# Kernel optimization log

Hardware: AMD Instinct MI355X
Metric: run time of the kernel (lower is better)

The kernel has to match this reference:

```python
import jax, jax.numpy as jnp
import numpy as np

NUM_NODES = 10000
WINDOW = 8
IN_C = 8
HID = 64
N_TOT = WINDOW * NUM_NODES
N_EDGES = 1280000
EPS = 1e-5


def setup_inputs() -> dict:
    key = jax.random.key(0)
    ks = jax.random.split(key, 12)
    s = 0.05
    X = jax.random.normal(ks[0], (N_TOT, IN_C), jnp.float32)
    edge_index = jax.random.randint(ks[1], (2, N_EDGES), 0, N_TOT, dtype=jnp.int32)
    edge_weight = jax.random.uniform(ks[2], (N_EDGES,), jnp.float32)
    return dict(
        X=X, edge_index=edge_index, edge_weight=edge_weight,
        w1=jax.random.normal(ks[3], (IN_C, HID), jnp.float32) * s, b1=jnp.zeros(HID, jnp.float32),
        w2=jax.random.normal(ks[4], (HID, HID), jnp.float32) * s, b2=jnp.zeros(HID, jnp.float32),
        g1=jnp.ones(HID, jnp.float32), be1=jnp.zeros(HID, jnp.float32),
        g2=jnp.ones(HID, jnp.float32), be2=jnp.zeros(HID, jnp.float32),
        wih1=jax.random.normal(ks[5], (4 * HID, 2 * HID), jnp.float32) * s,
        whh1=jax.random.normal(ks[6], (4 * HID, HID), jnp.float32) * s,
        bih1=jnp.zeros(4 * HID, jnp.float32), bhh1=jnp.zeros(4 * HID, jnp.float32),
        wih2=jax.random.normal(ks[7], (4 * HID, HID), jnp.float32) * s,
        whh2=jax.random.normal(ks[8], (4 * HID, HID), jnp.float32) * s,
        bih2=jnp.zeros(4 * HID, jnp.float32), bhh2=jnp.zeros(4 * HID, jnp.float32),
    )


def _gcn(x, src, dst, ew, w, b):
    h = x @ w
    deg = jax.ops.segment_sum(ew, dst, num_segments=N_TOT) + 1.0
    dinv = jax.lax.rsqrt(deg)
    norm = dinv[src] * ew * dinv[dst]                               # [E]
    agg = jax.ops.segment_sum(norm[:, None] * h[src], dst, num_segments=N_TOT)
    return agg + h * (dinv * dinv)[:, None] + b                      # self-loop term: h[i]/deg[i]


def _bn(x, g, b):
    # BatchNorm1d, training-mode batch statistics (biased variance)
    mu = x.mean(0)
    var = ((x - mu) ** 2).mean(0)
    return (x - mu) * jax.lax.rsqrt(var + EPS) * g + b


def _lstm(xs, wih, whh, bih, bhh):
    # xs: [T, B, F]; torch gate order i, f, g, o
    B = xs.shape[1]
    def step(carry, xt):
        h, c = carry
        z = xt @ wih.T + h @ whh.T + bih + bhh
        i, f, g, o = jnp.split(z, 4, axis=1)
        c = jax.nn.sigmoid(f) * c + jax.nn.sigmoid(i) * jnp.tanh(g)
        h = jax.nn.sigmoid(o) * jnp.tanh(c)
        return (h, c), h
    init = (jnp.zeros((B, HID), xs.dtype), jnp.zeros((B, HID), xs.dtype))
    (h, c), ys = jax.lax.scan(step, init, xs)
    return ys, h


def reference(X, edge_index, edge_weight, w1, b1, w2, b2, g1, be1, g2, be2,
              wih1, whh1, bih1, bhh1, wih2, whh2, bih2, bhh2):
    src, dst = edge_index[0], edge_index[1]
    # skip-feature S: [B*num_nodes, in_channels + window - 1]
    S = X.reshape(1, WINDOW, NUM_NODES, IN_C).transpose(0, 2, 1, 3).reshape(-1, WINDOW, IN_C)
    Sfeat = jnp.concatenate([S[:, 0, :], S[:, 1:, IN_C - 1]], axis=1)
    # two GCN layers (dropout omitted: deterministic baseline)
    x1 = _bn(jax.nn.relu(_gcn(X, src, dst, edge_weight, w1, b1)), g1, be1)
    x2 = _bn(jax.nn.relu(_gcn(x1, src, dst, edge_weight, w2, b2)), g2, be2)
    xc = jnp.concatenate([x1, x2], axis=1)                           # [N_TOT, 2H]
    xs = xc.reshape(1, WINDOW, NUM_NODES, 2 * HID).transpose(1, 0, 2, 3).reshape(WINDOW, -1, 2 * HID)
    ys, h1 = _lstm(xs, wih1, whh1, bih1, bhh1)
    ys2, h2 = _lstm(ys, wih2, whh2, bih2, bhh2)
    return jnp.concatenate([h1, h2, Sfeat], axis=1)                  # [num_nodes, 2H + IN_C + WINDOW - 1]
```

## Files before the change

kernel.cpp:

```cpp
#include <hip/hip_runtime.h>
#include <hip/hip_bf16.h>
#include <math.h>

#define NNODES 10000
#define NT     80000
#define NE     1280000
#define NBKT   625
#define CHUNK  5000
#define EPB    3072
#define BNEPS  1e-5f

typedef __bf16 bf16x8 __attribute__((ext_vector_type(8)));
typedef float  f32x4  __attribute__((ext_vector_type(4)));
typedef float  f32x2  __attribute__((ext_vector_type(2)));

__device__ __forceinline__ float frcp(float x){ return __builtin_amdgcn_rcpf(x); }
__device__ __forceinline__ float fsig(float x){ return frcp(1.0f + __expf(-x)); }
__device__ __forceinline__ float ftanh(float x){ return 1.0f - 2.0f*frcp(1.0f + __expf(2.0f*x)); }
__device__ __forceinline__ float u2f(unsigned int u){ union{unsigned int u; float f;} c; c.u=u; return c.f; }
__device__ __forceinline__ unsigned int f2u(float f){ union{float f; unsigned int u;} c; c.f=f; return c.u; }
__device__ __forceinline__ unsigned short f2bu(float v){ __hip_bfloat16 h = __float2bfloat16(v); return *(unsigned short*)&h; }
__device__ __forceinline__ unsigned int pk2(float a, float b){ return (unsigned int)f2bu(a) | ((unsigned int)f2bu(b) << 16); }
__device__ __forceinline__ float dec15(unsigned int p){ return u2f((p & 0x7fffu) << 17); }

__global__ __launch_bounds__(256) void prepA1_kernel(
    const int* __restrict__ dst, const float* __restrict__ X,
    unsigned int* __restrict__ Xb, int* __restrict__ histmat,
    const float* __restrict__ wih1, const float* __restrict__ whh1,
    const float* __restrict__ bih1, const float* __restrict__ bhh1,
    const float* __restrict__ wih2, const float* __restrict__ whh2,
    const float* __restrict__ bih2, const float* __restrict__ bhh2,
    const float* __restrict__ w1g, const float* __restrict__ w2g,
    unsigned int* __restrict__ W1f, unsigned int* __restrict__ W2f,
    float* __restrict__ bs1, float* __restrict__ bs2,
    unsigned int* __restrict__ W2g, unsigned int* __restrict__ W1g)
{
    __shared__ int h[NBKT];
    if (blockIdx.x < 256) {
        for (int i = threadIdx.x; i < NBKT; i += 256) h[i] = 0;
        __syncthreads();
        int base = blockIdx.x*CHUNK;
        for (int i = threadIdx.x; i < CHUNK; i += 256)
            atomicAdd(&h[dst[base + i] >> 7], 1);
        for (int i = threadIdx.x; i < 1250; i += 256) {
            int gid = blockIdx.x*1250 + i;
            float2 v = *(const float2*)&X[(size_t)gid*2];
            Xb[gid] = pk2(v.x, v.y);
        }
        __syncthreads();
        for (int i = threadIdx.x; i < NBKT; i += 256)
            histmat[blockIdx.x*640 + i] = h[i];
        return;
    }
    int gid = (blockIdx.x - 256)*256 + threadIdx.x;
    if (gid < 24576) {
        int i = gid & 3, lane = (gid>>2)&63, rest = gid>>8;
        int ks = rest % 6; rest /= 6;
        int nt = rest & 3, w = rest >> 2;
        int gate = nt*64 + w*16 + (lane & 15);
        int k = ks*32 + ((lane>>4)&3)*8 + 2*i;
        float v0 = (k     < 128) ? wih1[gate*128 + k]       : whh1[gate*64 + (k-128)];
        float v1 = (k + 1 < 128) ? wih1[gate*128 + k + 1]   : whh1[gate*64 + (k+1-128)];
        W1f[gid] = pk2(v0, v1);
    } else if (gid < 40960) {
        int r = gid - 24576;
        int i = r & 3, lane = (r>>2)&63, rest = r>>8;
        int ks = rest & 3; rest >>= 2;
        int nt = rest & 3, w = rest >> 2;
        int gate = nt*64 + w*16 + (lane & 15);
        int k = ks*32 + ((lane>>4)&3)*8 + 2*i;
        float v0 = (k     < 64) ? wih2[gate*64 + k]     : whh2[gate*64 + (k-64)];
        float v1 = (k + 1 < 64) ? wih2[gate*64 + k + 1] : whh2[gate*64 + (k+1-64)];
        W2f[r] = pk2(v0, v1);
    } else if (gid < 41216) {
        int j = gid - 40960; bs1[j] = bih1[j] + bhh1[j];
    } else if (gid < 41472) {
        int j = gid - 41216; bs2[j] = bih2[j] + bhh2[j];
    } else if (gid < 43520) {
        int r = gid - 41472;
        int i = r & 3, lane = (r>>2)&63, rest = r>>8;
        int ks = rest & 1, w = rest >> 1;
        int col = w*16 + (lane & 15);
        int k = ks*32 + ((lane>>4)&3)*8 + 2*i;
        W2g[r] = pk2(w2g[k*64 + col], w2g[(k+1)*64 + col]);
    } else if (gid < 44544) {
        int r = gid - 43520;
        int i = r & 3, lane = (r>>2)&63, w = r>>8;
        int col = w*16 + (lane & 15);
        int k = ((lane>>4)&3)*8 + 2*i;
        float v0 = (k     < 8) ? w1g[k*64 + col]     : 0.f;
        float v1 = (k + 1 < 8) ? w1g[(k+1)*64 + col] : 0.f;
        W1g[r] = pk2(v0, v1);
    }
}

__global__ __launch_bounds__(256) void sortA2a_kernel(const int* __restrict__ histmat,
                                                      int* __restrict__ offmatT,
                                                      int* __restrict__ binTotal)
{
    __shared__ int v[256];
    int b = blockIdx.x, t = threadIdx.x;
    int x = histmat[t*640 + b];
    v[t] = x;
    __syncthreads();
    for (int off = 1; off < 256; off <<= 1) {
        int y = (t >= off) ? v[t-off] : 0;
        __syncthreads();
        v[t] += y;
        __syncthreads();
    }
    offmatT[b*256 + t] = v[t] - x;
    if (t == 255) binTotal[b] = v[255];
}

__global__ __launch_bounds__(1024) void sortA2b_kernel(const int* __restrict__ binTotal,
                                                       int* __restrict__ bucketbase,
                                                       int* __restrict__ rowptr)
{
    __shared__ int part[1024];
    int t = threadIdx.x;
    int v = (t < NBKT) ? binTotal[t] : 0;
    part[t] = v;
    __syncthreads();
    for (int off = 1; off < 1024; off <<= 1) {
        int y = (t >= off) ? part[t-off] : 0;
        __syncthreads();
        part[t] += y;
        __syncthreads();
    }
    if (t < NBKT) bucketbase[t] = part[t] - v;
    if (t == 0) { bucketbase[NBKT] = NE; rowptr[NT] = NE; }
}

__global__ __launch_bounds__(256) void sortA3_kernel(const int* __restrict__ src,
                                                     const int* __restrict__ dst,
                                                     const float* __restrict__ ew,
                                                     const int* __restrict__ offmatT,
                                                     const int* __restrict__ bucketbase,
                                                     uint2* __restrict__ esort)
{
    __shared__ int cur[NBKT];
    int blk = blockIdx.x;
    for (int i = threadIdx.x; i < NBKT; i += 256)
        cur[i] = bucketbase[i] + offmatT[i*256 + blk];
    __syncthreads();
    int base = blk*CHUNK;
    for (int i = threadIdx.x; i < CHUNK; i += 256) {
        int e = base + i;
        int d = dst[e];
        int pos = atomicAdd(&cur[d >> 7], 1);
        uint2 r;
        r.x = (unsigned int)src[e] | ((unsigned int)(d & 127) << 17);
        r.y = f2u(ew[e]);
        esort[pos] = r;
    }
}

__global__ __launch_bounds__(256) void sortB1_kernel(const int* __restrict__ bucketbase,
                                                     const uint2* __restrict__ esort,
                                                     unsigned char* __restrict__ urank,
                                                     int* __restrict__ rowptr,
                                                     float* __restrict__ dinv)
{
    __shared__ int cnt[128];
    __shared__ float dg[128];
    __shared__ int ptr[128];
    int bin = blockIdx.x, t = threadIdx.x;
    if (t < 128) { cnt[t] = 0; dg[t] = 0.f; }
    __syncthreads();
    int base = bucketbase[bin], end = bucketbase[bin+1];
    for (int i = base + t; i < end; i += 256) {
        uint2 r = esort[i];
        int dl = (r.x >> 17) & 127;
        int rk = atomicAdd(&cnt[dl], 1);
        atomicAdd(&dg[dl], u2f(r.y));
        urank[i] = (unsigned char)rk;
    }
    __syncthreads();
    if (t < 128) ptr[t] = cnt[t];
    __syncthreads();
    for (int off = 1; off < 128; off <<= 1) {
        int y = (t >= off && t < 128) ? ptr[t-off] : 0;
        __syncthreads();
        if (t < 128) ptr[t] += y;
        __syncthreads();
    }
    if (t < 128) {
        rowptr[bin*128 + t] = base + ptr[t] - cnt[t];
        dinv[bin*128 + t]   = rsqrtf(dg[t] + 1.0f);
    }
}

__global__ __launch_bounds__(256) void sortB2g8m_kernel(const int* __restrict__ bucketbase,
                                                        const uint2* __restrict__ esort,
                                                        const unsigned char* __restrict__ urank,
                                                        const int* __restrict__ rowptr,
                                                        const float* __restrict__ dinv,
                                                        unsigned int* __restrict__ epack,
                                                        const uint4* __restrict__ Xb,
                                                        const unsigned int* __restrict__ W1g,
                                                        const float* __restrict__ b1,
                                                        unsigned short* __restrict__ y1,
                                                        float* __restrict__ sums)
{
    __shared__ unsigned int eld[EPB];
    __shared__ __align__(16) unsigned short As[128][8];
    __shared__ float smc[256][4], sqc[256][4];
    int bin = blockIdx.x;
    int base = bucketbase[bin], end = bucketbase[bin+1];
    int cnt = end - base;
    for (int i = threadIdx.x; i < cnt; i += 256) {
        uint2 r = esort[base + i];
        int s = r.x & 0x1FFFF;
        int d = bin*128 + ((r.x >> 17) & 127);
        float w = u2f(r.y) * dinv[s];
        unsigned int p15 = (f2u(w) + (1u << 16)) >> 17;
        unsigned int pv = ((unsigned int)s << 15) | p15;
        int pos = rowptr[d] + (int)urank[base + i];
        epack[pos] = pv;
        int lpos = pos - base;
        if (lpos < EPB) eld[lpos] = pv;
    }
    __syncthreads();
    {
        int t = threadIdx.x;
        int dl = t >> 1, par = t & 1;
        int d = bin*128 + dl;
        int beg = rowptr[d], endd = rowptr[d+1];
        float acc[8];
        #pragma unroll
        for (int k = 0; k < 8; ++k) acc[k] = 0.f;
        for (int i = beg + par; i < endd; i += 2) {
            int lpos = i - base;
            unsigned int p = (lpos < EPB) ? eld[lpos] : epack[i];
            float nrm = dec15(p);
            uint4 xv = Xb[p >> 15];
            unsigned int um[4] = {xv.x, xv.y, xv.z, xv.w};
            #pragma unroll
            for (int m = 0; m < 4; ++m) {
                acc[2*m]   = fmaf(nrm, u2f(um[m] << 16),         acc[2*m]);
                acc[2*m+1] = fmaf(nrm, u2f(um[m] & 0xffff0000u), acc[2*m+1]);
            }
        }
        #pragma unroll
        for (int k = 0; k < 8; ++k) acc[k] += __shfl_xor(acc[k], 1);
        if (par == 0) {
            float dv = dinv[d];
            uint4 xd = Xb[d];
            unsigned int ud[4] = {xd.x, xd.y, xd.z, xd.w};
            #pragma unroll
            for (int m = 0; m < 4; ++m) {
                acc[2*m]   = dv * fmaf(dv, u2f(ud[m] << 16),         acc[2*m]);
                acc[2*m+1] = dv * fmaf(dv, u2f(ud[m] & 0xffff0000u), acc[2*m+1]);
            }
            *(uint4*)&As[dl][0] = make_uint4(pk2(acc[0],acc[1]), pk2(acc[2],acc[3]),
                                             pk2(acc[4],acc[5]), pk2(acc[6],acc[7]));
        }
    }
    __syncthreads();
    {
        int t = threadIdx.x;
        int w = t >> 6, lane = t & 63, lr = lane & 15, lg = lane >> 4;
        uint4 bfrag[4];
        float bb[4];
        #pragma unroll
        for (int nt = 0; nt < 4; ++nt) {
            bfrag[nt] = ((const uint4*)W1g)[nt*64 + lane];
            bb[nt] = b1[nt*16 + lr];
        }
        float sc[4] = {0.f,0.f,0.f,0.f}, qc[4] = {0.f,0.f,0.f,0.f};
        #pragma unroll
        for (int rr = 0; rr < 2; ++rr) {
            int rt = w*2 + rr;
            bf16x8 a = {};
            if (lg == 0) a = *(const bf16x8*)&As[rt*16 + lr][0];
            #pragma unroll
            for (int nt = 0; nt < 4; ++nt) {
                union { uint4 u; bf16x8 v; } bw; bw.u = bfrag[nt];
                f32x4 acc = {0.f, 0.f, 0.f, 0.f};
                acc = __builtin_amdgcn_mfma_f32_16x16x32_bf16(a, bw.v, acc, 0, 0, 0);
                #pragma unroll
                for (int r = 0; r < 4; ++r) {
                    float v = fmaxf(acc[r] + bb[nt], 0.f);
                    int row = bin*128 + rt*16 + lg*4 + r;
                    y1[(size_t)row*64 + nt*16 + lr] = f2bu(v);
                    sc[nt] += v; qc[nt] += v*v;
                }
            }
        }
        #pragma unroll
        for (int nt = 0; nt < 4; ++nt) { smc[t][nt] = sc[nt]; sqc[t][nt] = qc[nt]; }
        __syncthreads();
        if (t < 64) {
            int nt = t >> 4, lr2 = t & 15;
            float s = 0.f, q = 0.f;
            #pragma unroll
            for (int w4 = 0; w4 < 4; ++w4)
                #pragma unroll
                for (int lg2 = 0; lg2 < 4; ++lg2) {
                    int idx = w4*64 + lg2*16 + lr2;
                    s += smc[idx][nt]; q += sqc[idx][nt];
                }
            atomicAdd(&sums[t], s);
            atomicAdd(&sums[64 + t], q);
        }
    }
}

__global__ __launch_bounds__(256) void xbn8_kernel(const unsigned int* __restrict__ y1,
                                                   const float* __restrict__ sums,
                                                   const float* __restrict__ g,
                                                   const float* __restrict__ be,
                                                   unsigned int* __restrict__ xcat,
                                                   unsigned int* __restrict__ x8)
{
    __shared__ float axs[64], bxs[64];
    int tid = threadIdx.x;
    if (tid < 64) {
        float mu  = sums[tid] * (1.0f/NT);
        float var = sums[64 + tid] * (1.0f/NT) - mu*mu;
        float a = rsqrtf(var + BNEPS) * g[tid];
        axs[tid] = a; bxs[tid] = be[tid] - mu*a;
    }
    __syncthreads();
    int gid = blockIdx.x*256 + tid;
    if (gid >= NT*16) return;
    int c4 = gid & 15, n = gid >> 4;
    int c0 = c4*4;
    uint2 yy = *(const uint2*)&y1[(size_t)n*32 + 2*c4];
    float v0 = fmaf(axs[c0+0], u2f(yy.x << 16),         bxs[c0+0]);
    float v1 = fmaf(axs[c0+1], u2f(yy.x & 0xffff0000u), bxs[c0+1]);
    float v2 = fmaf(axs[c0+2], u2f(yy.y << 16),         bxs[c0+2]);
    float v3 = fmaf(axs[c0+3], u2f(yy.y & 0xffff0000u), bxs[c0+3]);
    *(uint2*)&xcat[(size_t)n*64 + 2*c4] = make_uint2(pk2(v0, v1), pk2(v2, v3));
    int p8 = 0;
    p8 = __builtin_amdgcn_cvt_pk_fp8_f32(v0, v1, p8, false);
    p8 = __builtin_amdgcn_cvt_pk_fp8_f32(v2, v3, p8, true);
    x8[(size_t)n*16 + c4] = (unsigned int)p8;
}

__global__ __launch_bounds__(256) void gather64_kernel(const int* __restrict__ rowptr,
                                                       const unsigned int* __restrict__ epack,
                                                       const unsigned int* __restrict__ x8,
                                                       const float* __restrict__ dinv,
                                                       unsigned int* __restrict__ xcat)
{
    int lane = threadIdx.x & 63;
    int g = lane >> 3;
    int l = lane & 7;
    int gwave = blockIdx.x*4 + (threadIdx.x >> 6);
    int nwaves = gridDim.x*4;
    for (int dp = gwave; dp < NT/2; dp += nwaves) {
        int dA = dp*2, dB = dA + 1;
        int begA = rowptr[dA], endA = rowptr[dA+1];
        int begB = endA, endB = rowptr[dB+1];
        int nA = endA - begA, nB = endB - begB;
        int n = nA > nB ? nA : nB;
        int clA = (endA > begA) ? endA - 1 : 0;
        int clB = (endB > begB) ? endB - 1 : 0;
        float a0=0.f,a1=0.f,a2=0.f,a3=0.f,a4=0.f,a5=0.f,a6=0.f,a7=0.f;
        float b0=0.f,b1=0.f,b2=0.f,b3=0.f,b4=0.f,b5=0.f,b6=0.f,b7=0.f;
        for (int i = 0; i < n; i += 8) {
            int iA = begA + i + g;
            bool vA = iA < endA;
            unsigned int pA = epack[vA ? iA : clA];
            float nrmA = vA ? dec15(pA) : 0.f;
            int iB = begB + i + g;
            bool vB = iB < endB;
            unsigned int pB = epack[vB ? iB : clB];
            float nrmB = vB ? dec15(pB) : 0.f;
            uint2 xvA = *(const uint2*)&x8[(size_t)(pA >> 15)*16 + 2*l];
            uint2 xvB = *(const uint2*)&x8[(size_t)(pB >> 15)*16 + 2*l];
            f32x2 qa0 = __builtin_amdgcn_cvt_pk_f32_fp8((int)xvA.x, false);
            f32x2 qa1 = __builtin_amdgcn_cvt_pk_f32_fp8((int)xvA.x, true);
            f32x2 qa2 = __builtin_amdgcn_cvt_pk_f32_fp8((int)xvA.y, false);
            f32x2 qa3 = __builtin_amdgcn_cvt_pk_f32_fp8((int)xvA.y, true);
            a0 = fmaf(nrmA, qa0[0], a0); a1 = fmaf(nrmA, qa0[1], a1);
            a2 = fmaf(nrmA, qa1[0], a2); a3 = fmaf(nrmA, qa1[1], a3);
            a4 = fmaf(nrmA, qa2[0], a4); a5 = fmaf(nrmA, qa2[1], a5);
            a6 = fmaf(nrmA, qa3[0], a6); a7 = fmaf(nrmA, qa3[1], a7);
            f32x2 qb0 = __builtin_amdgcn_cvt_pk_f32_fp8((int)xvB.x, false);
            f32x2 qb1 = __builtin_amdgcn_cvt_pk_f32_fp8((int)xvB.x, true);
            f32x2 qb2 = __builtin_amdgcn_cvt_pk_f32_fp8((int)xvB.y, false);
            f32x2 qb3 = __builtin_amdgcn_cvt_pk_f32_fp8((int)xvB.y, true);
            b0 = fmaf(nrmB, qb0[0], b0); b1 = fmaf(nrmB, qb0[1], b1);
            b2 = fmaf(nrmB, qb1[0], b2); b3 = fmaf(nrmB, qb1[1], b3);
            b4 = fmaf(nrmB, qb2[0], b4); b5 = fmaf(nrmB, qb2[1], b5);
            b6 = fmaf(nrmB, qb3[0], b6); b7 = fmaf(nrmB, qb3[1], b7);
        }
        #pragma unroll
        for (int off = 8; off < 64; off <<= 1) {
            a0 += __shfl_xor(a0, off); a1 += __shfl_xor(a1, off);
            a2 += __shfl_xor(a2, off); a3 += __shfl_xor(a3, off);
            a4 += __shfl_xor(a4, off); a5 += __shfl_xor(a5, off);
            a6 += __shfl_xor(a6, off); a7 += __shfl_xor(a7, off);
            b0 += __shfl_xor(b0, off); b1 += __shfl_xor(b1, off);
            b2 += __shfl_xor(b2, off); b3 += __shfl_xor(b3, off);
            b4 += __shfl_xor(b4, off); b5 += __shfl_xor(b5, off);
            b6 += __shfl_xor(b6, off); b7 += __shfl_xor(b7, off);
        }
        if (g == 0) {
            float dvA = dinv[dA];
            uint4 xdA = *(const uint4*)&xcat[(size_t)dA*64 + 4*l];
            a0 = dvA * fmaf(dvA, u2f(xdA.x << 16),         a0);
            a1 = dvA * fmaf(dvA, u2f(xdA.x & 0xffff0000u), a1);
            a2 = dvA * fmaf(dvA, u2f(xdA.y << 16),         a2);
            a3 = dvA * fmaf(dvA, u2f(xdA.y & 0xffff0000u), a3);
            a4 = dvA * fmaf(dvA, u2f(xdA.z << 16),         a4);
            a5 = dvA * fmaf(dvA, u2f(xdA.z & 0xffff0000u), a5);
            a6 = dvA * fmaf(dvA, u2f(xdA.w << 16),         a6);
            a7 = dvA * fmaf(dvA, u2f(xdA.w & 0xffff0000u), a7);
            *(uint4*)&xcat[(size_t)dA*64 + 32 + 4*l] =
                make_uint4(pk2(a0,a1), pk2(a2,a3), pk2(a4,a5), pk2(a6,a7));
            float dvB = dinv[dB];
            uint4 xdB = *(const uint4*)&xcat[(size_t)dB*64 + 4*l];
            b0 = dvB * fmaf(dvB, u2f(xdB.x << 16),         b0);
            b1 = dvB * fmaf(dvB, u2f(xdB.x & 0xffff0000u), b1);
            b2 = dvB * fmaf(dvB, u2f(xdB.y << 16),         b2);
            b3 = dvB * fmaf(dvB, u2f(xdB.y & 0xffff0000u), b3);
            b4 = dvB * fmaf(dvB, u2f(xdB.z << 16),         b4);
            b5 = dvB * fmaf(dvB, u2f(xdB.z & 0xffff0000u), b5);
            b6 = dvB * fmaf(dvB, u2f(xdB.w << 16),         b6);
            b7 = dvB * fmaf(dvB, u2f(xdB.w & 0xffff0000u), b7);
            *(uint4*)&xcat[(size_t)dB*64 + 32 + 4*l] =
                make_uint4(pk2(b0,b1), pk2(b2,b3), pk2(b4,b5), pk2(b6,b7));
        }
    }
}

__global__ __launch_bounds__(256) void gemm64relu_kernel(const unsigned int* __restrict__ xcat,
                                                         const unsigned int* __restrict__ W2g,
                                                         const float* __restrict__ b,
                                                         unsigned short* __restrict__ y,
                                                         float* __restrict__ sums)
{
    __shared__ __align__(16) unsigned short As[64][72];
    __shared__ float sm[256], sq[256];
    const int tid = threadIdx.x;
    const int w = tid >> 6, lane = tid & 63, lr = lane & 15, lg = lane >> 4;
    union { uint4 u; bf16x8 v; } b0, b1;
    b0.u = ((const uint4*)W2g)[(w*2 + 0)*64 + lane];
    b1.u = ((const uint4*)W2g)[(w*2 + 1)*64 + lane];
    float bc = b[w*16 + lr];
    const int srow = tid >> 2, squad = tid & 3;
    float s = 0.f, q = 0.f;
    for (int tile = blockIdx.x; tile < NT/64; tile += gridDim.x) {
        int rbase = tile*64;
        __syncthreads();
        {
            const unsigned int* src = &xcat[(size_t)(rbase + srow)*64 + 32 + squad*8];
            unsigned int* dst = (unsigned int*)&As[srow][0] + squad*8;
            *(uint4*)(dst)     = *(const uint4*)(src);
            *(uint4*)(dst + 4) = *(const uint4*)(src + 4);
        }
        __syncthreads();
        #pragma unroll
        for (int rt = 0; rt < 4; ++rt) {
            bf16x8 a0 = *(const bf16x8*)&As[rt*16 + lr][lg*8];
            bf16x8 a1 = *(const bf16x8*)&As[rt*16 + lr][32 + lg*8];
            f32x4 acc = {0.f, 0.f, 0.f, 0.f};
            acc = __builtin_amdgcn_mfma_f32_16x16x32_bf16(a0, b0.v, acc, 0, 0, 0);
            acc = __builtin_amdgcn_mfma_f32_16x16x32_bf16(a1, b1.v, acc, 0, 0, 0);
            #pragma unroll
            for (int r = 0; r < 4; ++r) {
                float v = fmaxf(acc[r] + bc, 0.f);
                y[(size_t)(rbase + rt*16 + lg*4 + r)*64 + w*16 + lr] = f2bu(v);
                s += v; q += v*v;
            }
        }
    }
    sm[tid] = s; sq[tid] = q;
    __syncthreads();
    if (tid < 64) {
        int base = (tid >> 4)*64 + (tid & 15);
        atomicAdd(&sums[tid],      sm[base] + sm[base+16] + sm[base+32] + sm[base+48]);
        atomicAdd(&sums[64 + tid], sq[base] + sq[base+16] + sq[base+32] + sq[base+48]);
    }
}

#define LROW 328
__global__ __launch_bounds__(256, 2) void lstm_mfma_kernel(
    const unsigned int* __restrict__ xcat,
    const unsigned int* __restrict__ y2,
    const float* __restrict__ sums2, const float* __restrict__ g2,
    const float* __restrict__ be2,
    const unsigned int* __restrict__ W1f, const unsigned int* __restrict__ W2f,
    const float* __restrict__ bs1, const float* __restrict__ bs2,
    const float* __restrict__ X,
    float* __restrict__ out)
{
    __shared__ __align__(16) unsigned short xb[16][LROW];
    const int tid  = threadIdx.x;
    const int w    = tid >> 6, lane = tid & 63;
    const int lr   = lane & 15;
    const int lg   = lane >> 4;
    const int nb0  = blockIdx.x * 16;

    if (tid < 240) {
        int gid = blockIdx.x*240 + tid;
        int n = gid/15, ii = gid%15;
        float v = (ii < 8) ? X[(size_t)n*8 + ii]
                           : X[((size_t)(ii-7)*NNODES + n)*8 + 7];
        out[(size_t)n*143 + 128 + ii] = v;
    }

    uint4 w1f[4][6], w2f[4][4];
    {
        const uint4* p1 = (const uint4*)W1f;
        #pragma unroll
        for (int nt = 0; nt < 4; ++nt)
            #pragma unroll
            for (int ks = 0; ks < 6; ++ks)
                w1f[nt][ks] = p1[((w*4 + nt)*6 + ks)*64 + lane];
        const uint4* p2 = (const uint4*)W2f;
        #pragma unroll
        for (int nt = 0; nt < 4; ++nt)
            #pragma unroll
            for (int ks = 0; ks < 4; ++ks)
                w2f[nt][ks] = p2[((w*4 + nt)*4 + ks)*64 + lane];
    }
    float b1v[4], b2v[4];
    #pragma unroll
    for (int nt = 0; nt < 4; ++nt) {
        b1v[nt] = bs1[nt*64 + w*16 + lr];
        b2v[nt] = bs2[nt*64 + w*16 + lr];
    }

    const int sn = tid >> 4, k0 = (tid & 15)*8;
    float ax[8], bx[8];
    if (k0 >= 64) {
        #pragma unroll
        for (int j = 0; j < 8; ++j) {
            int c = k0 - 64 + j;
            float mu  = sums2[c] * (1.0f/NT);
            float var = sums2[64 + c] * (1.0f/NT) - mu*mu;
            float a = rsqrtf(var + BNEPS) * g2[c];
            ax[j] = a; bx[j] = be2[c] - mu*a;
        }
    }

    for (int i = tid; i < 16*24; i += 256) {
        int n = i / 24, kk = 128 + (i % 24)*8;
        uint4 z; z.x = z.y = z.z = z.w = 0u;
        *(uint4*)&xb[n][kk] = z;
    }

    auto stage = [&](int step) {
        size_t row = (size_t)(step*NNODES + nb0 + sn);
        uint4 raw;
        if (k0 < 64) {
            raw = *(const uint4*)&xcat[row*64 + (k0 >> 1)];
        } else {
            raw = *(const uint4*)&y2[row*32 + ((k0 - 64) >> 1)];
            unsigned int um[4] = {raw.x, raw.y, raw.z, raw.w};
            #pragma unroll
            for (int m = 0; m < 4; ++m) {
                float v0 = fmaf(ax[2*m],   u2f(um[m] << 16),         bx[2*m]);
                float v1 = fmaf(ax[2*m+1], u2f(um[m] & 0xffff0000u), bx[2*m+1]);
                um[m] = pk2(v0, v1);
            }
            raw.x = um[0]; raw.y = um[1]; raw.z = um[2]; raw.w = um[3];
        }
        *(uint4*)&xb[sn][k0] = raw;
    };
    stage(0);
    float c1[4] = {0.f,0.f,0.f,0.f}, c2[4] = {0.f,0.f,0.f,0.f};

    for (int step = 0; step < 8; ++step) {
        __syncthreads();

        f32x4 acc[4];
        #pragma unroll
        for (int nt = 0; nt < 4; ++nt) { acc[nt][0]=0.f; acc[nt][1]=0.f; acc[nt][2]=0.f; acc[nt][3]=0.f; }
        #pragma unroll
        for (int ks = 0; ks < 6; ++ks) {
            bf16x8 a = *(const bf16x8*)&xb[lr][ks*32 + lg*8];
            #pragma unroll
            for (int nt = 0; nt < 4; ++nt) {
                union { uint4 u; bf16x8 v; } wb; wb.u = w1f[nt][ks];
                acc[nt] = __builtin_amdgcn_mfma_f32_16x16x32_bf16(a, wb.v, acc[nt], 0, 0, 0);
            }
        }
        __syncthreads();

        #pragma unroll
        for (int r = 0; r < 4; ++r) {
            float zi = acc[0][r] + b1v[0];
            float zf = acc[1][r] + b1v[1];
            float zg = acc[2][r] + b1v[2];
            float zo = acc[3][r] + b1v[3];
            float c  = fsig(zf)*c1[r] + fsig(zi)*ftanh(zg);
            c1[r] = c;
            float hv = fsig(zo)*ftanh(c);
            int node = lg*4 + r;
            xb[node][128 + w*16 + lr] = f2bu(hv);
            if (step == 7) out[(size_t)(nb0 + node)*143 + w*16 + lr] = hv;
        }
        if (step < 7) stage(step + 1);
        __syncthreads();

        int rb = 192 + 64*((step+1)&1);
        int wb2 = 192 + 64*(step&1);
        #pragma unroll
        for (int nt = 0; nt < 4; ++nt) { acc[nt][0]=0.f; acc[nt][1]=0.f; acc[nt][2]=0.f; acc[nt][3]=0.f; }
        #pragma unroll
        for (int ks = 0; ks < 2; ++ks) {
            bf16x8 a = *(const bf16x8*)&xb[lr][128 + ks*32 + lg*8];
            #pragma unroll
            for (int nt = 0; nt < 4; ++nt) {
                union { uint4 u; bf16x8 v; } wbv; wbv.u = w2f[nt][ks];
                acc[nt] = __builtin_amdgcn_mfma_f32_16x16x32_bf16(a, wbv.v, acc[nt], 0, 0, 0);
            }
        }
        #pragma unroll
        for (int ks = 0; ks < 2; ++ks) {
            bf16x8 a = *(const bf16x8*)&xb[lr][rb + ks*32 + lg*8];
            #pragma unroll
            for (int nt = 0; nt < 4; ++nt) {
                union { uint4 u; bf16x8 v; } wbv; wbv.u = w2f[nt][2+ks];
                acc[nt] = __builtin_amdgcn_mfma_f32_16x16x32_bf16(a, wbv.v, acc[nt], 0, 0, 0);
            }
        }
        #pragma unroll
        for (int r = 0; r < 4; ++r) {
            float zi = acc[0][r] + b2v[0];
            float zf = acc[1][r] + b2v[1];
            float zg = acc[2][r] + b2v[2];
            float zo = acc[3][r] + b2v[3];
            float c  = fsig(zf)*c2[r] + fsig(zi)*ftanh(zg);
            c2[r] = c;
            float hv = fsig(zo)*ftanh(c);
            int node = lg*4 + r;
            xb[node][wb2 + w*16 + lr] = f2bu(hv);
            if (step == 7) out[(size_t)(nb0 + node)*143 + 64 + w*16 + lr] = hv;
        }
    }
}

extern "C" void kernel_launch(void* const* d_in, const int* in_sizes, int n_in,
                              void* d_out, int out_size, void* d_ws, size_t ws_size,
                              hipStream_t stream)
{
    (void)in_sizes; (void)n_in; (void)out_size; (void)ws_size;
    const float* X    = (const float*)d_in[0];
    const int*   ei   = (const int*)d_in[1];
    const float* ew   = (const float*)d_in[2];
    const float* w1   = (const float*)d_in[3];
    const float* b1   = (const float*)d_in[4];
    const float* w2   = (const float*)d_in[5];
    const float* b2   = (const float*)d_in[6];
    const float* g1   = (const float*)d_in[7];
    const float* be1  = (const float*)d_in[8];
    const float* g2   = (const float*)d_in[9];
    const float* be2  = (const float*)d_in[10];
    const float* wih1 = (const float*)d_in[11];
    const float* whh1 = (const float*)d_in[12];
    const float* bih1 = (const float*)d_in[13];
    const float* bhh1 = (const float*)d_in[14];
    const float* wih2 = (const float*)d_in[15];
    const float* whh2 = (const float*)d_in[16];
    const float* bih2 = (const float*)d_in[17];
    const float* bhh2 = (const float*)d_in[18];
    float* out = (float*)d_out;
    float* ws  = (float*)d_ws;

    const int* src = ei;
    const int* dst = ei + NE;

    float* sums      = ws;
    float* dinv      = ws + 256;
    int*   rowptr    = (int*)(ws + 80256);
    int*   binTotal  = (int*)(ws + 160260);
    int*   bucketbase= (int*)(ws + 160900);
    int*   histmat   = (int*)(ws + 161540);
    int*   offmatT   = (int*)(ws + 325380);
    unsigned char* urank = (unsigned char*)(ws + 485380);
    uint2* esort     = (uint2*)(ws + 805384);
    unsigned int* x8 = (unsigned int*)(ws + 805384);
    unsigned int* y2 = (unsigned int*)(ws + 805384);
    unsigned int* epack = (unsigned int*)(ws + 3365384);
    unsigned int* Xb = (unsigned int*)(ws + 4645384);
    unsigned int* y1 = (unsigned int*)(ws + 5605384);
    unsigned int* xcat = (unsigned int*)(ws + 8165384);
    unsigned int* W1f  = (unsigned int*)(ws + 13285384);
    unsigned int* W2f  = W1f + 24576;
    float* bs1 = (float*)(W2f + 16384);
    float* bs2 = bs1 + 256;
    unsigned int* W2g  = (unsigned int*)(bs2 + 256);
    unsigned int* W1g  = W2g + 2048;

    hipMemsetAsync(ws, 0, 256 * 4, stream);

    prepA1_kernel<<<430, 256, 0, stream>>>(dst, X, Xb, histmat,
                                           wih1,whh1,bih1,bhh1,
                                           wih2,whh2,bih2,bhh2,
                                           w1, w2,
                                           W1f,W2f,bs1,bs2,W2g,W1g);
    sortA2a_kernel<<<NBKT, 256, 0, stream>>>(histmat, offmatT, binTotal);
    sortA2b_kernel<<<1, 1024, 0, stream>>>(binTotal, bucketbase, rowptr);
    sortA3_kernel<<<256, 256, 0, stream>>>(src, dst, ew, offmatT, bucketbase, esort);
    sortB1_kernel<<<NBKT, 256, 0, stream>>>(bucketbase, esort, urank, rowptr, dinv);
    sortB2g8m_kernel<<<NBKT, 256, 0, stream>>>(bucketbase, esort, urank, rowptr, dinv,
                                               epack, (const uint4*)Xb, W1g, b1,
                                               (unsigned short*)y1, sums);

    xbn8_kernel<<<(NT*16+255)/256, 256, 0, stream>>>(y1, sums, g1, be1, xcat, x8);

    gather64_kernel<<<2048, 256, 0, stream>>>(rowptr, epack, x8, dinv, xcat);
    gemm64relu_kernel<<<320, 256, 0, stream>>>(xcat, W2g, b2, (unsigned short*)y2, sums + 128);

    lstm_mfma_kernel<<<NNODES/16, 256, 0, stream>>>(xcat, y2, sums + 128, g2, be2,
                                                    W1f, W2f, bs1, bs2, X, out);
}
```

Measured before the change: 174.9 us.

## Fuse bucket scans via last-block atomic and gather four rows per wave

Merges the two-kernel scan (per-bucket scan plus a single-block scan of the bucket totals) into one kernel. The last block to finish, found with an atomic counter, does the final scan, which removes one launch and the dependency gap between kernels. The gather kernel now handles four destination rows per wave instead of two, which raises memory-level parallelism on the irregular fp8 gathers. In exchange it uses more registers, and load imbalance can grow because the loop runs to the longest of four rows.

```diff
diff --git a/kernel.cpp b/kernel.cpp
--- a/kernel.cpp
+++ b/kernel.cpp
@@ -94,11 +94,15 @@
     }
 }
 
-__global__ __launch_bounds__(256) void sortA2a_kernel(const int* __restrict__ histmat,
-                                                      int* __restrict__ offmatT,
-                                                      int* __restrict__ binTotal)
+__global__ __launch_bounds__(256) void sortA2_kernel(const int* __restrict__ histmat,
+                                                     int* __restrict__ offmatT,
+                                                     int* __restrict__ binTotal,
+                                                     int* __restrict__ donecnt,
+                                                     int* __restrict__ bucketbase,
+                                                     int* __restrict__ rowptr)
 {
     __shared__ int v[256];
+    __shared__ int amlast;
     int b = blockIdx.x, t = threadIdx.x;
     int x = histmat[t*640 + b];
     v[t] = x;
@@ -111,24 +115,32 @@
     }
     offmatT[b*256 + t] = v[t] - x;
     if (t == 255) binTotal[b] = v[255];
-}
-
-__global__ __launch_bounds__(1024) void sortA2b_kernel(const int* __restrict__ binTotal,
-                                                       int* __restrict__ bucketbase,
-                                                       int* __restrict__ rowptr)
-{
-    __shared__ int part[1024];
-    int t = threadIdx.x;
-    int v = (t < NBKT) ? binTotal[t] : 0;
-    part[t] = v;
-    __syncthreads();
-    for (int off = 1; off < 1024; off <<= 1) {
-        int y = (t >= off) ? part[t-off] : 0;
-        __syncthreads();
-        part[t] += y;
-        __syncthreads();
-    }
-    if (t < NBKT) bucketbase[t] = part[t] - v;
+    __syncthreads();
+    if (t == 0) {
+        __threadfence();
+        int old = __hip_atomic_fetch_add(donecnt, 1, __ATOMIC_ACQ_REL,
+                                         __HIP_MEMORY_SCOPE_AGENT);
+        amlast = (old == NBKT - 1);
+    }
+    __syncthreads();
+    if (!amlast) return;
+    int b3 = 3*t;
+    int v0 = (b3     < NBKT) ? binTotal[b3]     : 0;
+    int v1 = (b3 + 1 < NBKT) ? binTotal[b3 + 1] : 0;
+    int v2 = (b3 + 2 < NBKT) ? binTotal[b3 + 2] : 0;
+    int s = v0 + v1 + v2;
+    v[t] = s;
+    __syncthreads();
+    for (int off = 1; off < 256; off <<= 1) {
+        int y = (t >= off) ? v[t-off] : 0;
+        __syncthreads();
+        v[t] += y;
+        __syncthreads();
+    }
+    int ex = v[t] - s;
+    if (b3     < NBKT) bucketbase[b3]     = ex;
+    if (b3 + 1 < NBKT) bucketbase[b3 + 1] = ex + v0;
+    if (b3 + 2 < NBKT) bucketbase[b3 + 2] = ex + v0 + v1;
     if (t == 0) { bucketbase[NBKT] = NE; rowptr[NT] = NE; }
 }
 
@@ -350,80 +362,70 @@
     int l = lane & 7;
     int gwave = blockIdx.x*4 + (threadIdx.x >> 6);
     int nwaves = gridDim.x*4;
-    for (int dp = gwave; dp < NT/2; dp += nwaves) {
-        int dA = dp*2, dB = dA + 1;
-        int begA = rowptr[dA], endA = rowptr[dA+1];
-        int begB = endA, endB = rowptr[dB+1];
-        int nA = endA - begA, nB = endB - begB;
-        int n = nA > nB ? nA : nB;
-        int clA = (endA > begA) ? endA - 1 : 0;
-        int clB = (endB > begB) ? endB - 1 : 0;
-        float a0=0.f,a1=0.f,a2=0.f,a3=0.f,a4=0.f,a5=0.f,a6=0.f,a7=0.f;
-        float b0=0.f,b1=0.f,b2=0.f,b3=0.f,b4=0.f,b5=0.f,b6=0.f,b7=0.f;
+    for (int dp = gwave; dp < NT/4; dp += nwaves) {
+        int d0 = dp*4;
+        int rp[5];
+        #pragma unroll
+        for (int q = 0; q < 5; ++q) rp[q] = rowptr[d0 + q];
+        int n = 0;
+        #pragma unroll
+        for (int q = 0; q < 4; ++q) { int c = rp[q+1] - rp[q]; if (c > n) n = c; }
+        float acc[4][8];
+        #pragma unroll
+        for (int q = 0; q < 4; ++q)
+            #pragma unroll
+            for (int k = 0; k < 8; ++k) acc[q][k] = 0.f;
         for (int i = 0; i < n; i += 8) {
-            int iA = begA + i + g;
-            bool vA = iA < endA;
-            unsigned int pA = epack[vA ? iA : clA];
-            float nrmA = vA ? dec15(pA) : 0.f;
-            int iB = begB + i + g;
-            bool vB = iB < endB;
-            unsigned int pB = epack[vB ? iB : clB];
-            float nrmB = vB ? dec15(pB) : 0.f;
-            uint2 xvA = *(const uint2*)&x8[(size_t)(pA >> 15)*16 + 2*l];
-            uint2 xvB = *(const uint2*)&x8[(size_t)(pB >> 15)*16 + 2*l];
-            f32x2 qa0 = __builtin_amdgcn_cvt_pk_f32_fp8((int)xvA.x, false);
-            f32x2 qa1 = __builtin_amdgcn_cvt_pk_f32_fp8((int)xvA.x, true);
-            f32x2 qa2 = __builtin_amdgcn_cvt_pk_f32_fp8((int)xvA.y, false);
-            f32x2 qa3 = __builtin_amdgcn_cvt_pk_f32_fp8((int)xvA.y, true);
-            a0 = fmaf(nrmA, qa0[0], a0); a1 = fmaf(nrmA, qa0[1], a1);
-            a2 = fmaf(nrmA, qa1[0], a2); a3 = fmaf(nrmA, qa1[1], a3);
-            a4 = fmaf(nrmA, qa2[0], a4); a5 = fmaf(nrmA, qa2[1], a5);
-            a6 = fmaf(nrmA, qa3[0], a6); a7 = fmaf(nrmA, qa3[1], a7);
-            f32x2 qb0 = __builtin_amdgcn_cvt_pk_f32_fp8((int)xvB.x, false);
-            f32x2 qb1 = __builtin_amdgcn_cvt_pk_f32_fp8((int)xvB.x, true);
-            f32x2 qb2 = __builtin_amdgcn_cvt_pk_f32_fp8((int)xvB.y, false);
-            f32x2 qb3 = __builtin_amdgcn_cvt_pk_f32_fp8((int)xvB.y, true);
-            b0 = fmaf(nrmB, qb0[0], b0); b1 = fmaf(nrmB, qb0[1], b1);
-            b2 = fmaf(nrmB, qb1[0], b2); b3 = fmaf(nrmB, qb1[1], b3);
-            b4 = fmaf(nrmB, qb2[0], b4); b5 = fmaf(nrmB, qb2[1], b5);
-            b6 = fmaf(nrmB, qb3[0], b6); b7 = fmaf(nrmB, qb3[1], b7);
-        }
-        #pragma unroll
-        for (int off = 8; off < 64; off <<= 1) {
-            a0 += __shfl_xor(a0, off); a1 += __shfl_xor(a1, off);
-            a2 += __shfl_xor(a2, off); a3 += __shfl_xor(a3, off);
-            a4 += __shfl_xor(a4, off); a5 += __shfl_xor(a5, off);
-            a6 += __shfl_xor(a6, off); a7 += __shfl_xor(a7, off);
-            b0 += __shfl_xor(b0, off); b1 += __shfl_xor(b1, off);
-            b2 += __shfl_xor(b2, off); b3 += __shfl_xor(b3, off);
-            b4 += __shfl_xor(b4, off); b5 += __shfl_xor(b5, off);
-            b6 += __shfl_xor(b6, off); b7 += __shfl_xor(b7, off);
-        }
+            #pragma unroll
+            for (int q = 0; q < 4; ++q) {
+                int idx = rp[q] + i + g;
+                bool valid = idx < rp[q+1];
+                int cl = (rp[q+1] > rp[q]) ? rp[q+1] - 1 : 0;
+                unsigned int p = epack[valid ? idx : cl];
+                float nrm = valid ? dec15(p) : 0.f;
+                uint2 xv = *(const uint2*)&x8[(size_t)(p >> 15)*16 + 2*l];
+                f32x2 q0 = __builtin_amdgcn_cvt_pk_f32_fp8((int)xv.x, false);
+                f32x2 q1 = __builtin_amdgcn_cvt_pk_f32_fp8((int)xv.x, true);
+                f32x2 q2 = __builtin_amdgcn_cvt_pk_f32_fp8((int)xv.y, false);
+                f32x2 q3 = __builtin_amdgcn_cvt_pk_f32_fp8((int)xv.y, true);
+                acc[q][0] = fmaf(nrm, q0[0], acc[q][0]);
+                acc[q][1] = fmaf(nrm, q0[1], acc[q][1]);
+                acc[q][2] = fmaf(nrm, q1[0], acc[q][2]);
+                acc[q][3] = fmaf(nrm, q1[1], acc[q][3]);
+                acc[q][4] = fmaf(nrm, q2[0], acc[q][4]);
+                acc[q][5] = fmaf(nrm, q2[1], acc[q][5]);
+                acc[q][6] = fmaf(nrm, q3[0], acc[q][6]);
+                acc[q][7] = fmaf(nrm, q3[1], acc[q][7]);
+            }
+        }
+        #pragma unroll
+        for (int off = 8; off < 64; off <<= 1)
+            #pragma unroll
+            for (int q = 0; q < 4; ++q)
+                #pragma unroll
+                for (int k = 0; k < 8; ++k)
+                    acc[q][k] += __shfl_xor(acc[q][k], off);
         if (g == 0) {
-            float dvA = dinv[dA];
-            uint4 xdA = *(const uint4*)&xcat[(size_t)dA*64 + 4*l];
-            a0 = dvA * fmaf(dvA, u2f(xdA.x << 16),         a0);
-            a1 = dvA * fmaf(dvA, u2f(xdA.x & 0xffff0000u), a1);
-            a2 = dvA * fmaf(dvA, u2f(xdA.y << 16),         a2);
-            a3 = dvA * fmaf(dvA, u2f(xdA.y & 0xffff0000u), a3);
-            a4 = dvA * fmaf(dvA, u2f(xdA.z << 16),         a4);
-            a5 = dvA * fmaf(dvA, u2f(xdA.z & 0xffff0000u), a5);
-            a6 = dvA * fmaf(dvA, u2f(xdA.w << 16),         a6);
-            a7 = dvA * fmaf(dvA, u2f(xdA.w & 0xffff0000u), a7);
-            *(uint4*)&xcat[(size_t)dA*64 + 32 + 4*l] =
-                make_uint4(pk2(a0,a1), pk2(a2,a3), pk2(a4,a5), pk2(a6,a7));
-            float dvB = dinv[dB];
-            uint4 xdB = *(const uint4*)&xcat[(size_t)dB*64 + 4*l];
-            b0 = dvB * fmaf(dvB, u2f(xdB.x << 16),         b0);
-            b1 = dvB * fmaf(dvB, u2f(xdB.x & 0xffff0000u), b1);
-            b2 = dvB * fmaf(dvB, u2f(xdB.y << 16),         b2);
-            b3 = dvB * fmaf(dvB, u2f(xdB.y & 0xffff0000u), b3);
-            b4 = dvB * fmaf(dvB, u2f(xdB.z << 16),         b4);
-            b5 = dvB * fmaf(dvB, u2f(xdB.z & 0xffff0000u), b5);
-            b6 = dvB * fmaf(dvB, u2f(xdB.w << 16),         b6);
-            b7 = dvB * fmaf(dvB, u2f(xdB.w & 0xffff0000u), b7);
-            *(uint4*)&xcat[(size_t)dB*64 + 32 + 4*l] =
-                make_uint4(pk2(b0,b1), pk2(b2,b3), pk2(b4,b5), pk2(b6,b7));
+            #pragma unroll
+            for (int q = 0; q < 4; ++q) {
+                int d = d0 + q;
+                float dv = dinv[d];
+                uint4 xd = *(const uint4*)&xcat[(size_t)d*64 + 4*l];
+                float x0 = u2f(xd.x << 16), x1 = u2f(xd.x & 0xffff0000u);
+                float x2 = u2f(xd.y << 16), x3 = u2f(xd.y & 0xffff0000u);
+                float x4 = u2f(xd.z << 16), x5 = u2f(xd.z & 0xffff0000u);
+                float x6 = u2f(xd.w << 16), x7 = u2f(xd.w & 0xffff0000u);
+                float r0 = dv * fmaf(dv, x0, acc[q][0]);
+                float r1 = dv * fmaf(dv, x1, acc[q][1]);
+                float r2 = dv * fmaf(dv, x2, acc[q][2]);
+                float r3 = dv * fmaf(dv, x3, acc[q][3]);
+                float r4 = dv * fmaf(dv, x4, acc[q][4]);
+                float r5 = dv * fmaf(dv, x5, acc[q][5]);
+                float r6 = dv * fmaf(dv, x6, acc[q][6]);
+                float r7 = dv * fmaf(dv, x7, acc[q][7]);
+                *(uint4*)&xcat[(size_t)d*64 + 32 + 4*l] =
+                    make_uint4(pk2(r0,r1), pk2(r2,r3), pk2(r4,r5), pk2(r6,r7));
+            }
         }
     }
 }
@@ -668,13 +670,14 @@
     const int* dst = ei + NE;
 
     float* sums      = ws;
-    float* dinv      = ws + 256;
-    int*   rowptr    = (int*)(ws + 80256);
-    int*   binTotal  = (int*)(ws + 160260);
-    int*   bucketbase= (int*)(ws + 160900);
-    int*   histmat   = (int*)(ws + 161540);
-    int*   offmatT   = (int*)(ws + 325380);
-    unsigned char* urank = (unsigned char*)(ws + 485380);
+    int*   donecnt   = (int*)(ws + 256);
+    float* dinv      = ws + 260;
+    int*   rowptr    = (int*)(ws + 80260);
+    int*   binTotal  = (int*)(ws + 160264);
+    int*   bucketbase= (int*)(ws + 160904);
+    int*   histmat   = (int*)(ws + 161544);
+    int*   offmatT   = (int*)(ws + 325384);
+    unsigned char* urank = (unsigned char*)(ws + 485384);
     uint2* esort     = (uint2*)(ws + 805384);
     unsigned int* x8 = (unsigned int*)(ws + 805384);
     unsigned int* y2 = (unsigned int*)(ws + 805384);
@@ -689,15 +692,15 @@
     unsigned int* W2g  = (unsigned int*)(bs2 + 256);
     unsigned int* W1g  = W2g + 2048;
 
-    hipMemsetAsync(ws, 0, 256 * 4, stream);
+    hipMemsetAsync(ws, 0, 260 * 4, stream);
 
     prepA1_kernel<<<430, 256, 0, stream>>>(dst, X, Xb, histmat,
                                            wih1,whh1,bih1,bhh1,
                                            wih2,whh2,bih2,bhh2,
                                            w1, w2,
                                            W1f,W2f,bs1,bs2,W2g,W1g);
-    sortA2a_kernel<<<NBKT, 256, 0, stream>>>(histmat, offmatT, binTotal);
-    sortA2b_kernel<<<1, 1024, 0, stream>>>(binTotal, bucketbase, rowptr);
+    sortA2_kernel<<<NBKT, 256, 0, stream>>>(histmat, offmatT, binTotal, donecnt,
+                                            bucketbase, rowptr);
     sortA3_kernel<<<256, 256, 0, stream>>>(src, dst, ew, offmatT, bucketbase, esort);
     sortB1_kernel<<<NBKT, 256, 0, stream>>>(bucketbase, esort, urank, rowptr, dinv);
     sortB2g8m_kernel<<<NBKT, 256, 0, stream>>>(bucketbase, esort, urank, rowptr, dinv,
```

Result: slower. 200.4 us (+14.6%).
